# Performance work log

Measured on AMD Instinct MI355X. Metric: run time of the kernel, lower is better.

## Reference

```python
import jax, jax.numpy as jnp
from jax import lax
import numpy as np

WIDTH = 3.0        # tool half-width (voxels)
SIGMA = 1.0        # soft mask edge (voxels)
BLUR_SIGMA = 1.5   # post-deposit isotropic blur sigma (voxels)
EPS = 1e-8


def _gauss_blur(x, sigma):
    """Separable Gaussian blur over the last two axes of x: [B, X, Y]."""
    radius = int(3 * sigma)
    t = jnp.arange(-radius, radius + 1, dtype=x.dtype)
    k = jnp.exp(-0.5 * (t / sigma) ** 2)
    k = k / k.sum()
    x4 = x[:, None]                      # [B,1,X,Y] NCHW
    kh = k.reshape(1, 1, -1, 1)
    x4 = lax.conv_general_dilated(x4, kh, (1, 1), 'SAME')
    kw = k.reshape(1, 1, 1, -1)
    x4 = lax.conv_general_dilated(x4, kw, (1, 1), 'SAME')
    return x4[:, 0]


def setup_inputs() -> dict:
    key = jax.random.key(0)
    k1, k2, k3 = jax.random.split(key, 3)
    B, H, W = 16, 1024, 1024
    occ = jax.random.uniform(k1, (B, H, W), dtype=jnp.float32)
    # push start/end points well inside the grid (voxel coordinates)
    action_start = jax.random.uniform(k2, (B, 3), minval=200.0, maxval=800.0, dtype=jnp.float32)
    action_end = action_start + jax.random.uniform(k3, (B, 3), minval=-150.0, maxval=150.0, dtype=jnp.float32)
    return {"occ": occ, "action_start": action_start, "action_end": action_end}


def reference(occ, action_start, action_end):
    # coordinate-convention transpose (see SplatPushModel docs)
    rho = jnp.swapaxes(occ, 1, 2)            # [B, X, Y]
    B, X, Y = rho.shape
    p0 = action_start[:, :2]                 # [B,2]
    p1 = action_end[:, :2]                   # [B,2]

    d = p1 - p0
    L = jnp.sqrt(jnp.sum(d * d, axis=-1) + EPS)      # [B] segment length
    u = d / L[:, None]                               # unit push direction
    n = jnp.stack([-u[:, 1], u[:, 0]], axis=-1)      # unit normal

    gx = jnp.arange(X, dtype=rho.dtype)[None, :, None]   # [1,X,1]
    gy = jnp.arange(Y, dtype=rho.dtype)[None, None, :]   # [1,1,Y]
    bc = lambda v: v[:, None, None]                      # [B] -> [B,1,1]

    # --- swept band: soft distance-to-segment mask ---
    rx = gx - bc(p0[:, 0])
    ry = gy - bc(p0[:, 1])
    t = jnp.clip(rx * bc(u[:, 0]) + ry * bc(u[:, 1]), 0.0, L[:, None, None])
    dx = rx - t * bc(u[:, 0])
    dy = ry - t * bc(u[:, 1])
    dist = jnp.sqrt(dx * dx + dy * dy + EPS)
    swept = jax.nn.sigmoid((WIDTH - dist) / SIGMA)       # [B,X,Y]

    m_swept = jnp.sum(rho * swept, axis=(1, 2))          # [B] mass to move
    pile_depth = m_swept / (2.0 * WIDTH)                 # [B]

    # --- landing zone probe (rectangle past p1) ---
    qx = gx - bc(p1[:, 0])
    qy = gy - bc(p1[:, 1])
    s = qx * bc(u[:, 0]) + qy * bc(u[:, 1])              # along-direction coord
    r = qx * bc(n[:, 0]) + qy * bc(n[:, 1])              # perpendicular coord
    lat = jax.nn.sigmoid((WIDTH - jnp.abs(r)) / SIGMA)
    probe = jax.nn.sigmoid(s / SIGMA) * jax.nn.sigmoid((bc(pile_depth) - s) / SIGMA) * lat
    existing = jnp.sum(rho * probe, axis=(1, 2))         # [B]
    extra = existing / (2.0 * WIDTH)                     # [B] forward extension

    # --- deposit band, shifted forward by extra_depth ---
    dep_mask = (jax.nn.sigmoid((s - bc(extra)) / SIGMA)
                * jax.nn.sigmoid((bc(extra) + bc(pile_depth) - s) / SIGMA)
                * lat)
    dep_norm = m_swept / (jnp.sum(dep_mask, axis=(1, 2)) + EPS)
    dep = dep_mask * dep_norm[:, None, None]             # mass-conserving deposit

    if BLUR_SIGMA > 0:
        dep = _gauss_blur(dep, BLUR_SIGMA)

    rho_new = rho * (1.0 - swept) + dep
    return jnp.swapaxes(rho_new, 1, 2)
```

## Files before the change

### kernel.cpp

```cpp
#include <hip/hip_runtime.h>
#include <math.h>

#define BB    16
#define HH    1024
#define WW    1024
#define EPSF  1e-8f
#define RAD   4
#define MARG  24.f
#define NB1   128
#define NB3   32
#define WMAX  128
#define FW    (WMAX + 16)

struct BlurK { float k[9]; };

__device__ __forceinline__ float sigf(float z) {
    z = fmaxf(fminf(z, 40.f), -40.f);
    return 1.f / (1.f + __expf(-z));
}

struct Geom { float p0x, p0y, p1x, p1y, L, ux, uy; };

__device__ __forceinline__ Geom load_geom(const float* as, const float* ae, int b) {
    Geom g;
    g.p0x = as[3 * b];  g.p0y = as[3 * b + 1];
    g.p1x = ae[3 * b];  g.p1y = ae[3 * b + 1];
    float dx = g.p1x - g.p0x, dy = g.p1y - g.p0y;
    g.L  = sqrtf(dx * dx + dy * dy + EPSF);
    g.ux = dx / g.L;  g.uy = dy / g.L;
    return g;
}

__device__ __forceinline__ float sweptf(const Geom& g, float x, float y) {
    float rx = x - g.p0x, ry = y - g.p0y;
    float t  = fminf(fmaxf(rx * g.ux + ry * g.uy, 0.f), g.L);
    float dx = rx - t * g.ux, dy = ry - t * g.uy;
    float dist = sqrtf(dx * dx + dy * dy + EPSF);
    return sigf(3.f - dist);
}

__device__ __forceinline__ void slat(const Geom& g, float x, float y, float& s, float& lat) {
    float qx = x - g.p1x, qy = y - g.p1y;
    s = qx * g.ux + qy * g.uy;
    float r = qx * (-g.uy) + qy * g.ux;
    lat = sigf(3.f - fabsf(r));
}

__device__ __forceinline__ void capsule_bbox(const Geom& g, float m,
                                             int& x0, int& x1, int& y0, int& y1) {
    x0 = max(0, (int)floorf(fminf(g.p0x, g.p1x) - m));
    x1 = min(WW - 1, (int)ceilf(fmaxf(g.p0x, g.p1x) + m));
    y0 = max(0, (int)floorf(fminf(g.p0y, g.p1y) - m));
    y1 = min(HH - 1, (int)ceilf(fmaxf(g.p0y, g.p1y) + m));
}

__device__ __forceinline__ void strip_bbox(const Geom& g, float s0, float s1, float m,
                                           int& x0, int& x1, int& y0, int& y1) {
    float xmin = 1e9f, xmax = -1e9f, ymin = 1e9f, ymax = -1e9f;
    #pragma unroll
    for (int i = 0; i < 4; i++) {
        float s = (i & 1) ? s1 : s0;
        float r = (i & 2) ? m : -m;
        float x = g.p1x + s * g.ux - r * g.uy;
        float y = g.p1y + s * g.uy + r * g.ux;
        xmin = fminf(xmin, x); xmax = fmaxf(xmax, x);
        ymin = fminf(ymin, y); ymax = fmaxf(ymax, y);
    }
    x0 = max(0, (int)floorf(xmin)); x1 = min(WW - 1, (int)ceilf(xmax));
    y0 = max(0, (int)floorf(ymin)); y1 = min(HH - 1, (int)ceilf(ymax));
}

__device__ __forceinline__ bool ivx(float a, float A, float B, float& lo, float& hi) {
    if (fabsf(a) < 1e-5f) return !(A > 0.f || B < 0.f);
    float l = A / a, h = B / a;
    if (a < 0.f) { float t = l; l = h; h = t; }
    lo = fmaxf(lo, l); hi = fminf(hi, h);
    return true;
}

__device__ __forceinline__ bool row_clip(const Geom& g, float fy, float sA, float sB,
                                         int& xa, int& xb) {
    const float dy = fy - g.p1y;
    float lo = -1e9f, hi = 1e9f;
    bool ok = ivx(g.ux, sA - dy * g.uy, sB - dy * g.uy, lo, hi);
    ok = ok && ivx(-g.uy, -MARG - dy * g.ux, MARG - dy * g.ux, lo, hi);
    if (!ok || lo > hi) return false;
    xa = max(0, (int)floorf(lo + g.p1x));
    xb = min(WW - 1, (int)ceilf(hi + g.p1x));
    return xa <= xb;
}

__device__ __forceinline__ float brb256(float v, float* sm) {
    #pragma unroll
    for (int off = 32; off > 0; off >>= 1) v += __shfl_down(v, off);
    const int lane = threadIdx.x & 63, wid = threadIdx.x >> 6;
    if (lane == 0) sm[wid] = v;
    __syncthreads();
    float r = sm[0] + sm[1] + sm[2] + sm[3];
    __syncthreads();
    return r;
}

__global__ __launch_bounds__(256)
void k_main(const float* __restrict__ occ, const float* __restrict__ as,
            const float* __restrict__ ae, float* __restrict__ out,
            float* __restrict__ part1) {
    const int b = blockIdx.y, bx = blockIdx.x, tid = threadIdx.x;
    Geom g = load_geom(as, ae, b);
    const size_t ibase = (size_t)b << 20;
    const float4* src = (const float4*)(occ + ibase);
    float4*       dst = (float4*)(out + ibase);
    const int yb = bx * 8;
    const int base4 = bx * 2048 + tid;

    float4 v[8];
    #pragma unroll
    for (int k = 0; k < 8; k++) v[k] = src[base4 + k * 256];

    int cx0, cx1, cy0, cy1; capsule_bbox(g, MARG, cx0, cx1, cy0, cy1);
    const int x = tid << 2;
    float msum = 0.f;
    if (x + 3 >= cx0 && x <= cx1) {
        #pragma unroll
        for (int k = 0; k < 8; k++) {
            const int y = yb + k;
            if (y >= cy0 && y <= cy1) {
                const float fy = (float)y, fx = (float)x;
                const float s0 = sweptf(g, fx + 0.f, fy);
                const float s1 = sweptf(g, fx + 1.f, fy);
                const float s2 = sweptf(g, fx + 2.f, fy);
                const float s3 = sweptf(g, fx + 3.f, fy);
                msum += v[k].x * s0 + v[k].y * s1 + v[k].z * s2 + v[k].w * s3;
                v[k].x *= 1.f - s0; v[k].y *= 1.f - s1;
                v[k].z *= 1.f - s2; v[k].w *= 1.f - s3;
            }
        }
    }
    #pragma unroll
    for (int k = 0; k < 8; k++) dst[base4 + k * 256] = v[k];

    __shared__ float sm[4];
    const float bs = brb256(msum, sm);
    if (tid == 0) part1[b * NB1 + bx] = bs;
}

__global__ __launch_bounds__(256)
void k_dep(const float* __restrict__ occ, const float* __restrict__ as,
           const float* __restrict__ ae, const float* __restrict__ part1,
           float* __restrict__ out, BlurK wk) {
    const int b = blockIdx.y, bx = blockIdx.x, tid = threadIdx.x;
    const int lane = tid & 63, wv = tid >> 6;
    __shared__ float sm[4];
    Geom g = load_geom(as, ae, b);
    const float* ob = occ + ((size_t)b << 20);

    const float m_swept = brb256((tid < NB1) ? part1[b * NB1 + tid] : 0.f, sm);
    const float pile = m_swept * (1.f / 6.f);

    int x0, x1, y0, y1;
    strip_bbox(g, -MARG, pile + MARG, MARG, x0, x1, y0, y1);
    float sum = 0.f;
    for (int y = y0 + wv; y <= y1; y += 4) {
        const float fy = (float)y;
        int xa, xb;
        if (!row_clip(g, fy, -MARG, pile + MARG, xa, xb)) continue;
        for (int xx = xa + lane; xx <= xb; xx += 64) {
            float s, lat; slat(g, (float)xx, fy, s, lat);
            sum += ob[((size_t)y << 10) + xx] * sigf(s) * sigf(pile - s) * lat;
        }
    }
    const float existing = brb256(sum, sm);
    const float extra = existing * (1.f / 6.f);

    const float sA = extra - MARG, sB = extra + pile + MARG;
    int sx0, sx1, sy0, sy1;
    strip_bbox(g, sA, sB, MARG, sx0, sx1, sy0, sy1);
    sum = 0.f;
    for (int y = sy0 + wv; y <= sy1; y += 4) {
        const float fy = (float)y;
        int xa, xb;
        if (!row_clip(g, fy, sA, sB, xa, xb)) continue;
        for (int xx = xa + lane; xx <= xb; xx += 64) {
            float s, lat; slat(g, (float)xx, fy, s, lat);
            sum += sigf(s - extra) * sigf(extra + pile - s) * lat;
        }
    }
    const float summask = brb256(sum, sm);
    const float dep_norm = m_swept / (summask + EPSF);

    if (sx0 > sx1 || sy0 > sy1) return;
    float* outb = out + ((size_t)b << 20);

    __shared__ float draw[16][FW];
    __shared__ float hb[16][WMAX];

    const int nty = (sy1 - sy0) / 8 + 1;

    for (int ty = bx; ty < nty; ty += NB3) {
        const int yt = sy0 + ty * 8;

        float xlo = 1e9f, xhi = -1e9f;
        #pragma unroll
        for (int r = 0; r < 16; r++) {
            const float dy = (float)(yt - RAD + r) - g.p1y;
            float lo = -1e9f, hi = 1e9f;
            bool ok = ivx(g.ux, sA - dy * g.uy, sB - dy * g.uy, lo, hi);
            ok = ok && ivx(-g.uy, -MARG - dy * g.ux, MARG - dy * g.ux, lo, hi);
            if (ok && lo <= hi) { xlo = fminf(xlo, lo); xhi = fmaxf(xhi, hi); }
        }
        const int csx0 = max(sx0, (int)floorf(xlo + g.p1x));
        const int csx1 = min(sx1, (int)ceilf(xhi + g.p1x));
        if (csx0 > csx1) continue;

        for (int cx = csx0 & ~3; cx <= csx1; cx += WMAX) {
            const int w = min(WMAX, csx1 - cx + 1);

            for (int i = tid; i < 16 * FW; i += 256) {
                const int ly = i / FW, lx = i - ly * FW;
                if (lx < w + 8) {
                    const int gy = yt - RAD + ly, gx = cx - RAD + lx;
                    float val = 0.f;
                    if ((unsigned)gx < WW && (unsigned)gy < HH) {
                        float s, lat; slat(g, (float)gx, (float)gy, s, lat);
                        val = sigf(s - extra) * sigf(extra + pile - s) * lat * dep_norm;
                    }
                    draw[ly][lx] = val;
                }
            }
            __syncthreads();

            for (int i = tid; i < 16 * WMAX; i += 256) {
                const int ly = i >> 7, lx = i & 127;
                if (lx < w) {
                    float acc = 0.f;
                    #pragma unroll
                    for (int j = 0; j < 9; j++) acc += wk.k[j] * draw[ly][lx + j];
                    hb[ly][lx] = acc;
                }
            }
            __syncthreads();

            for (int i = tid; i < 8 * WMAX; i += 256) {
                const int k = i >> 7, lx = i & 127;
                if (lx < w) {
                    float acc = 0.f;
                    #pragma unroll
                    for (int j = 0; j < 9; j++) acc += wk.k[j] * hb[k + j][lx];
                    draw[k][lx] = acc;
                }
            }
            __syncthreads();

            for (int i = tid; i < 8 * WMAX; i += 256) {
                const int k = i >> 7, lx = i & 127;
                const int gy = yt + k, gx = cx + lx;
                if (lx < w && (unsigned)gy < HH && (unsigned)gx < WW)
                    outb[((size_t)gy << 10) + gx] += draw[k][lx];
            }
            __syncthreads();
        }
    }
}

extern "C" void kernel_launch(void* const* d_in, const int* in_sizes, int n_in,
                              void* d_out, int out_size, void* d_ws, size_t ws_size,
                              hipStream_t stream) {
    const float* occ = (const float*)d_in[0];
    const float* as  = (const float*)d_in[1];
    const float* ae  = (const float*)d_in[2];
    float* out   = (float*)d_out;
    float* part1 = (float*)d_ws;

    BlurK wk;
    {
        float s = 0.f;
        for (int i = 0; i < 9; i++) {
            float t = (float)(i - RAD) / 1.5f;
            wk.k[i] = expf(-0.5f * t * t);
            s += wk.k[i];
        }
        for (int i = 0; i < 9; i++) wk.k[i] /= s;
    }

    k_main<<<dim3(NB1, BB), 256, 0, stream>>>(occ, as, ae, out, part1);
    k_dep <<<dim3(NB3, BB), 256, 0, stream>>>(occ, as, ae, part1, out, wk);
}
```

Measured before the change: 167.6 us.

## Split landing-zone probe reduction into separate multi-block kernel

Moves the landing-zone probe sum out of the deposit kernel into a new kernel that spreads the reduction over 64 blocks per batch and writes partial sums to workspace. The deposit kernel then just reduces these partials instead of having every block redundantly recompute the full probe sum. This removes redundant per-block work and parallelism limits, at the cost of an extra launch and scanning the full bounding box without per-row clipping.

```diff
diff --git a/kernel.cpp b/kernel.cpp
--- a/kernel.cpp
+++ b/kernel.cpp
@@ -8,6 +8,7 @@
 #define RAD   4
 #define MARG  24.f
 #define NB1   128
+#define NB2   64
 #define NB3   32
 #define WMAX  128
 #define FW    (WMAX + 16)
@@ -145,37 +146,47 @@
 }
 
 __global__ __launch_bounds__(256)
-void k_dep(const float* __restrict__ occ, const float* __restrict__ as,
-           const float* __restrict__ ae, const float* __restrict__ part1,
+void k_existing(const float* __restrict__ occ, const float* __restrict__ as,
+                const float* __restrict__ ae, const float* __restrict__ part1,
+                float* __restrict__ part2) {
+    const int b = blockIdx.y, bx = blockIdx.x, tid = threadIdx.x;
+    __shared__ float sm[4];
+    const float m_swept = brb256((tid < NB1) ? part1[b * NB1 + tid] : 0.f, sm);
+    const float pile = m_swept * (1.f / 6.f);
+
+    Geom g = load_geom(as, ae, b);
+    int x0, x1, y0, y1; strip_bbox(g, -MARG, pile + MARG, MARG, x0, x1, y0, y1);
+    const float* base = occ + ((size_t)b << 20);
+    float sum = 0.f;
+    for (int y = y0 + bx; y <= y1; y += NB2) {
+        const float fy = (float)y;
+        for (int x = x0 + tid; x <= x1; x += 256) {
+            float s, lat; slat(g, (float)x, fy, s, lat);
+            sum += base[((size_t)y << 10) + x] * sigf(s) * sigf(pile - s) * lat;
+        }
+    }
+    const float bs = brb256(sum, sm);
+    if (tid == 0) part2[b * NB2 + bx] = bs;
+}
+
+__global__ __launch_bounds__(256)
+void k_dep(const float* __restrict__ as, const float* __restrict__ ae,
+           const float* __restrict__ part1, const float* __restrict__ part2,
            float* __restrict__ out, BlurK wk) {
     const int b = blockIdx.y, bx = blockIdx.x, tid = threadIdx.x;
     const int lane = tid & 63, wv = tid >> 6;
     __shared__ float sm[4];
     Geom g = load_geom(as, ae, b);
-    const float* ob = occ + ((size_t)b << 20);
-
-    const float m_swept = brb256((tid < NB1) ? part1[b * NB1 + tid] : 0.f, sm);
-    const float pile = m_swept * (1.f / 6.f);
-
-    int x0, x1, y0, y1;
-    strip_bbox(g, -MARG, pile + MARG, MARG, x0, x1, y0, y1);
-    float sum = 0.f;
-    for (int y = y0 + wv; y <= y1; y += 4) {
-        const float fy = (float)y;
-        int xa, xb;
-        if (!row_clip(g, fy, -MARG, pile + MARG, xa, xb)) continue;
-        for (int xx = xa + lane; xx <= xb; xx += 64) {
-            float s, lat; slat(g, (float)xx, fy, s, lat);
-            sum += ob[((size_t)y << 10) + xx] * sigf(s) * sigf(pile - s) * lat;
-        }
-    }
-    const float existing = brb256(sum, sm);
+
+    const float m_swept  = brb256((tid < NB1) ? part1[b * NB1 + tid] : 0.f, sm);
+    const float existing = brb256((tid < NB2) ? part2[b * NB2 + tid] : 0.f, sm);
+    const float pile  = m_swept * (1.f / 6.f);
     const float extra = existing * (1.f / 6.f);
 
     const float sA = extra - MARG, sB = extra + pile + MARG;
     int sx0, sx1, sy0, sy1;
     strip_bbox(g, sA, sB, MARG, sx0, sx1, sy0, sy1);
-    sum = 0.f;
+    float sum = 0.f;
     for (int y = sy0 + wv; y <= sy1; y += 4) {
         const float fy = (float)y;
         int xa, xb;
@@ -270,6 +281,7 @@
     const float* ae  = (const float*)d_in[2];
     float* out   = (float*)d_out;
     float* part1 = (float*)d_ws;
+    float* part2 = part1 + BB * NB1;
 
     BlurK wk;
     {
@@ -282,6 +294,7 @@
         for (int i = 0; i < 9; i++) wk.k[i] /= s;
     }
 
-    k_main<<<dim3(NB1, BB), 256, 0, stream>>>(occ, as, ae, out, part1);
-    k_dep <<<dim3(NB3, BB), 256, 0, stream>>>(occ, as, ae, part1, out, wk);
-}
+    k_main    <<<dim3(NB1, BB), 256, 0, stream>>>(occ, as, ae, out, part1);
+    k_existing<<<dim3(NB2, BB), 256, 0, stream>>>(occ, as, ae, part1, part2);
+    k_dep     <<<dim3(NB3, BB), 256, 0, stream>>>(as, ae, part1, part2, out, wk);
+}
```

Measured after the change: 150.5 us. 10.2% less time.
